# Kernel tuning notes

Hardware: AMD Instinct MI355X
Metric: run time of the kernel (lower is better)

The kernel has to match this reference:

```python
import jax, jax.numpy as jnp
import numpy as np

# Per-species MLP dims from CoefficientLayer._create_model (H, C, N, O), aev_dim=384
DIMS = {"h": [384, 160, 128, 96, 1], "c": [384, 144, 112, 96, 1], "n": [384, 128, 112, 96, 1], "o": [384, 128, 112, 96, 1]}


def setup_inputs() -> dict:
    key = jax.random.key(0)
    B, A, D = 256, 256, 384
    ks = jax.random.split(key, 64)
    inp = {}
    inp["species"] = jax.random.randint(ks[0], (B, A), 0, 4)  # species index 0..3
    inp["aev"] = jax.random.normal(ks[1], (B, A, D), dtype=jnp.float32)
    inp["b0"] = jnp.array([0.1, 0.2, 0.3, 0.4], dtype=jnp.float32)  # shifter intercepts
    inp["b1"] = jnp.array([1.0, 1.1, 0.9, 1.2], dtype=jnp.float32)  # shifter slopes
    ki = 2
    for name, dims in DIMS.items():
        for l in range(4):
            fi, fo = dims[l], dims[l + 1]
            inp[f"{name}w{l}"] = jax.random.normal(ks[ki], (fi, fo), dtype=jnp.float32) / np.float32(np.sqrt(fi))
            ki += 1
            inp[f"{name}b{l}"] = jnp.zeros((fo,), dtype=jnp.float32)
    return inp


def _mlp(x, ws, bs):
    # Linear -> CELU(0.1) x3 -> Linear(->1), squeeze last dim
    for i in range(3):
        x = jax.nn.celu(x @ ws[i] + bs[i], alpha=0.1)
    return (x @ ws[3] + bs[3])[..., 0]


def reference(species, aev, b0, b1,
              hw0, hb0, hw1, hb1, hw2, hb2, hw3, hb3,
              cw0, cb0, cw1, cb1, cw2, cb2, cw3, cb3,
              nw0, nb0, nw1, nb1, nw2, nb2, nw3, nb3,
              ow0, ob0, ow1, ob1, ow2, ob2, ow3, ob3):
    nets = [
        ([hw0, hw1, hw2, hw3], [hb0, hb1, hb2, hb3]),
        ([cw0, cw1, cw2, cw3], [cb0, cb1, cb2, cb3]),
        ([nw0, nw1, nw2, nw3], [nb0, nb1, nb2, nb3]),
        ([ow0, ow1, ow2, ow3], [ob0, ob1, ob2, ob3]),
    ]
    # ANIModel hard routing: each atom's coefficient comes from its species' network;
    # atoms with species == -1 (padding) stay 0.
    coef = jnp.zeros(species.shape, dtype=aev.dtype)
    for i, (ws, bs) in enumerate(nets):  # fixed small loop over 4 species
        coef = jnp.where(species == i, _mlp(aev, ws, bs), coef)
    # Shifter: result[mask_i] = b0[i] + b1[i] * coef[mask_i]; padding stays 0
    idx = jnp.clip(species, 0)
    return jnp.where(species >= 0, b0[idx] + b1[idx] * coef, jnp.zeros((), dtype=aev.dtype))
```

## Files before the change

kernel.cpp:

```cpp
#include <hip/hip_runtime.h>

typedef _Float16 f16;
typedef _Float16 f16x4 __attribute__((ext_vector_type(4)));
typedef _Float16 f16x8 __attribute__((ext_vector_type(8)));
typedef float f32x4 __attribute__((ext_vector_type(4)));
typedef unsigned short u16;
typedef unsigned int u32;

#define NATOMS 65536
#define CAP 17920

#define WS_LISTS_OFF 256
#define WS_W_OFF 524544
#define WS_W_ELEMS 350208
#define WS_NEEDED (WS_W_OFF + WS_W_ELEMS * 2)

#define BLKF 64

#define ROWB 1536
#define ROWH 768
#define TILEH 12288

struct ConvJob { const float* src; int K, N, KS, NT, CK, off; };

struct PrepParams {
  const int* species;
  int* counts;
  u16* lists;
  f16* wbase;
  ConvJob jobs[16];
};

struct GemmParams {
  const float* aev;
  const float* b0;
  const float* b1;
  const float* bias[4][4];
  const float* w3src[4];
  const f16* w[4][4];
  const int* counts;
  const u16* lists;
  float* out;
  int Nreal0[4];
  int Nreal1[4];
};

template <int N> struct AF { f16x8 v[N]; };

__global__ __launch_bounds__(256) void prep_kernel(PrepParams p) {
  int tid = threadIdx.x;
  if (blockIdx.x < 256) {
    __shared__ int wcnt[4][4];
    __shared__ int wbase[4][4];
    int i = blockIdx.x * 256 + tid;
    int s = p.species[i];
    int wave = tid >> 6, lane = tid & 63;
    unsigned long long m[4];
    #pragma unroll
    for (int t = 0; t < 4; t++) {
      m[t] = __ballot(s == t);
      if (lane == 0) wcnt[wave][t] = __popcll(m[t]);
    }
    __syncthreads();
    if (tid < 4) {
      int t = tid;
      int c0 = wcnt[0][t], c1 = wcnt[1][t], c2 = wcnt[2][t], c3 = wcnt[3][t];
      int base = atomicAdd(&p.counts[t], c0 + c1 + c2 + c3);
      wbase[0][t] = base;
      wbase[1][t] = base + c0;
      wbase[2][t] = base + c0 + c1;
      wbase[3][t] = base + c0 + c1 + c2;
    }
    __syncthreads();
    int rnk = __popcll(m[s] & ((1ull << lane) - 1ull));
    p.lists[s * NATOMS + wbase[wave][s] + rnk] = (u16)i;
  } else {
    int bx = blockIdx.x - 256;
    int job = bx / 30, bxin = bx - job * 30;
    ConvJob jb = p.jobs[job];
    int e = bxin * 256 + tid;
    int nslots = jb.KS * jb.NT * 64;
    if (e >= nslots) return;
    int frag = e >> 6, lane = e & 63;
    int c = frag / (jb.CK * jb.NT);
    int rem = frag - c * (jb.CK * jb.NT);
    int ckc = min(jb.CK, jb.KS - c * jb.CK);
    int nt = rem / ckc, ki = rem - nt * ckc;
    int ks = c * jb.CK + ki;
    int q = lane >> 4, nlo = lane & 15;
    int n = nt * 16 + nlo;
    int k0 = ks * 32 + q * 8;
    f16x8 v;
    #pragma unroll
    for (int j = 0; j < 8; j++) {
      int k = k0 + j;
      float x = (n < jb.N && k < jb.K) ? jb.src[k * jb.N + n] : 0.f;
      v[j] = (f16)x;
    }
    *(f16x8*)(p.wbase + jb.off + (size_t)e * 8) = v;
  }
}

__device__ __forceinline__ float celu01(float v) {
  return v > 0.f ? v : 0.1f * (__expf(v * 10.f) - 1.f);
}

__device__ __forceinline__ void stage_frag(const f16* g, f16* l, int lane) {
  __builtin_amdgcn_global_load_lds(
      (const __attribute__((address_space(1))) u32*)(g + lane * 8),
      (__attribute__((address_space(3))) u32*)l, 16, 0, 0);
}

template <int NT0, int KS1>
__device__ void fused_body(const GemmParams& p, int s, int bl, char* smem) {
  constexpr int LDSA_OFF = 4 * TILEH;
  constexpr int TSTRIDE = 16 * 168;
  constexpr int W1_OFF = LDSA_OFF + 8 * TSTRIDE * 2;
  constexpr int W2_OFF = W1_OFF + 40 * 512 * 2;
  constexpr int ATOMS_OFF = W2_OFF + 24 * 512 * 2;
  constexpr int NF1 = KS1 * 8;

  int tid = threadIdx.x, w = tid >> 6, lane = tid & 63;
  int q = lane >> 4, nlo = lane & 15;
  int cnt = min(p.counts[s], CAP);
  int ntiles = (cnt + 15) >> 4;
  int tpb = (ntiles + BLKF - 1) / BLKF;
  int t0 = bl * tpb;
  int nt_blk = min(ntiles - t0, tpb);
  if (nt_blk <= 0) return;

  f16* ldsA = (f16*)(smem + LDSA_OFF);
  f16* W1 = (f16*)(smem + W1_OFF);
  f16* W2 = (f16*)(smem + W2_OFF);
  u16* atoms_l = (u16*)(smem + ATOMS_OFF);

  const f16* g1 = p.w[s][1];
  const f16* g2 = p.w[s][2];
  for (int f = w; f < NF1 + 24; f += 10) {
    if (f < NF1) stage_frag(g1 + (size_t)f * 512, W1 + f * 512, lane);
    else stage_frag(g2 + (size_t)(f - NF1) * 512, W2 + (f - NF1) * 512, lane);
  }

  f16x8 wf[12];
  float bvv[4];
  if (w < NT0) {
    const f16* wg = p.w[s][0];
    #pragma unroll
    for (int ks = 0; ks < 12; ks++)
      wf[ks] = *(const f16x8*)(wg + (size_t)(ks * NT0 + w) * 512 + lane * 8);
    #pragma unroll
    for (int r = 0; r < 4; r++) {
      int n = w * 16 + q * 4 + r;
      bvv[r] = (n < p.Nreal0[s]) ? p.bias[s][0][n] : 0.f;
    }
  }

  int Nr1 = p.Nreal1[s];
  const float* bias1 = p.bias[s][1];
  const float* bias2 = p.bias[s][2];
  const float* w3 = p.w3src[s];
  float bv1[8], b2v[6], w3v[6];
  #pragma unroll
  for (int nt = 0; nt < 8; nt++) {
    int n = nt * 16 + nlo;
    bv1[nt] = (n < Nr1) ? bias1[n] : 0.f;
  }
  #pragma unroll
  for (int nt = 0; nt < 6; nt++) {
    int n = nt * 16 + nlo;
    b2v[nt] = bias2[n];
    w3v[nt] = w3[n];
  }
  float b3 = p.bias[s][3][0];
  float b0v = p.b0[s], b1v = p.b1[s];

  const u16* list = p.lists + s * NATOMS;
  for (int idx = tid; idx < nt_blk * 16; idx += 640)
    atoms_l[idx] = list[min(t0 * 16 + idx, cnt - 1)];
  __syncthreads();

  bool stager = (w < 8);
  int frow[3], fintra[3];
  #pragma unroll
  for (int j = 0; j < 3; j++) {
    int o32 = (w + 8 * j) * 1024 + lane * 16;
    frow[j] = o32 / ROWB;
    fintra[j] = o32 - frow[j] * ROWB;
  }

  f32x4 ldA[3], ldB[3];
  auto issueA = [&](int i) {
    #pragma unroll
    for (int j = 0; j < 3; j++) {
      int atom = atoms_l[i * 16 + frow[j]];
      ldA[j] = *(const f32x4*)((const char*)p.aev + (size_t)atom * ROWB + fintra[j]);
    }
  };
  auto issueB = [&](int i) {
    #pragma unroll
    for (int j = 0; j < 3; j++) {
      int atom = atoms_l[i * 16 + frow[j]];
      ldB[j] = *(const f32x4*)((const char*)p.aev + (size_t)atom * ROWB + fintra[j]);
    }
  };
  auto writeA = [&](int i) {
    char* buf = smem + (i & 3) * TILEH;
    #pragma unroll
    for (int j = 0; j < 3; j++) {
      int o16 = (w + 8 * j) * 512 + lane * 8;
      int addr = o16 ^ ((frow[j] & 7) << 4);
      f16x4 h = {(f16)ldA[j][0], (f16)ldA[j][1], (f16)ldA[j][2], (f16)ldA[j][3]};
      *(f16x4*)(buf + addr) = h;
    }
  };
  auto writeB = [&](int i) {
    char* buf = smem + (i & 3) * TILEH;
    #pragma unroll
    for (int j = 0; j < 3; j++) {
      int o16 = (w + 8 * j) * 512 + lane * 8;
      int addr = o16 ^ ((frow[j] & 7) << 4);
      f16x4 h = {(f16)ldB[j][0], (f16)ldB[j][1], (f16)ldB[j][2], (f16)ldB[j][3]};
      *(f16x4*)(buf + addr) = h;
    }
  };
  auto computeT = [&](int i, int lo) {
    const char* buf = smem + (i & 3) * TILEH;
    int swz = (nlo & 7) << 4;
    int base = nlo * ROWH + q * 16;
    f32x4 acc = {0.f, 0.f, 0.f, 0.f};
    #pragma unroll
    for (int ks = 0; ks < 12; ks++) {
      f16x8 a = *(const f16x8*)(buf + ((base + ks * 64) ^ swz));
      acc = __builtin_amdgcn_mfma_f32_16x16x32_f16(wf[ks], a, acc, 0, 0, 0);
    }
    f16* A = ldsA + (i - lo) * TSTRIDE;
    f16x4 o;
    #pragma unroll
    for (int r = 0; r < 4; r++) o[r] = (f16)celu01(acc[r] + bvv[r]);
    *(f16x4*)(A + nlo * 168 + w * 16 + q * 4) = o;
  };

  for (int lo = 0; lo < nt_blk; lo += 8) {
    int hi = min(nt_blk, lo + 8);

    if (stager) {
      issueA(lo);
      if (lo + 1 < hi) issueB(lo + 1);
      writeA(lo);
      if (lo + 1 < hi) writeB(lo + 1);
      if (lo + 2 < hi) issueA(lo + 2);
      if (lo + 3 < hi) issueB(lo + 3);
    }
    asm volatile("s_waitcnt lgkmcnt(0)" ::: "memory");
    __builtin_amdgcn_s_barrier();

    for (int i = lo; i < hi; i += 2) {
      if (stager) {
        if (i + 2 < hi) writeA(i + 2);
        if (i + 3 < hi) writeB(i + 3);
        if (i + 4 < hi) issueA(i + 4);
        if (i + 5 < hi) issueB(i + 5);
      }
      if (w < NT0) {
        computeT(i, lo);
        if (i + 1 < hi) computeT(i + 1, lo);
      }
      asm volatile("s_waitcnt lgkmcnt(0)" ::: "memory");
      __builtin_amdgcn_s_barrier();
    }

    if (w < 8 && lo + w < hi) {
      int i = lo + w;
      f16* A = ldsA + w * TSTRIDE;
      AF<KS1> a1;
      #pragma unroll
      for (int ks = 0; ks < KS1; ks++)
        a1.v[ks] = *(const f16x8*)(A + nlo * 168 + ks * 32 + q * 8);
      f32x4 acc1[8];
      #pragma unroll
      for (int nt = 0; nt < 8; nt++) acc1[nt] = f32x4{0.f, 0.f, 0.f, 0.f};
      #pragma unroll
      for (int ks = 0; ks < KS1; ks++) {
        #pragma unroll
        for (int nt = 0; nt < 8; nt++) {
          f16x8 b = *(const f16x8*)(W1 + (ks * 8 + nt) * 512 + lane * 8);
          acc1[nt] = __builtin_amdgcn_mfma_f32_16x16x32_f16(a1.v[ks], b, acc1[nt], 0, 0, 0);
        }
      }
      #pragma unroll
      for (int nt = 0; nt < 8; nt++) {
        #pragma unroll
        for (int r = 0; r < 4; r++)
          A[(q * 4 + r) * 168 + nt * 16 + nlo] = (f16)celu01(acc1[nt][r] + bv1[nt]);
      }
      AF<4> a2;
      #pragma unroll
      for (int ks = 0; ks < 4; ks++)
        a2.v[ks] = *(const f16x8*)(A + nlo * 168 + ks * 32 + q * 8);
      f32x4 acc2[6];
      #pragma unroll
      for (int nt = 0; nt < 6; nt++) acc2[nt] = f32x4{0.f, 0.f, 0.f, 0.f};
      #pragma unroll
      for (int ks = 0; ks < 4; ks++) {
        #pragma unroll
        for (int nt = 0; nt < 6; nt++) {
          f16x8 b = *(const f16x8*)(W2 + (ks * 6 + nt) * 512 + lane * 8);
          acc2[nt] = __builtin_amdgcn_mfma_f32_16x16x32_f16(a2.v[ks], b, acc2[nt], 0, 0, 0);
        }
      }
      float pr[4] = {0.f, 0.f, 0.f, 0.f};
      #pragma unroll
      for (int nt = 0; nt < 6; nt++) {
        #pragma unroll
        for (int r = 0; r < 4; r++) {
          float v = celu01(acc2[nt][r] + b2v[nt]);
          pr[r] += v * w3v[nt];
        }
      }
      #pragma unroll
      for (int m = 1; m < 16; m <<= 1) {
        #pragma unroll
        for (int r = 0; r < 4; r++) pr[r] += __shfl_xor(pr[r], m);
      }
      if (nlo == 0) {
        #pragma unroll
        for (int r = 0; r < 4; r++) {
          int row = (t0 + i) * 16 + q * 4 + r;
          if (row < cnt)
            p.out[atoms_l[i * 16 + q * 4 + r]] = b0v + b1v * (pr[r] + b3);
        }
      }
    }
    asm volatile("s_waitcnt lgkmcnt(0)" ::: "memory");
    __builtin_amdgcn_s_barrier();
  }
}

__global__ __launch_bounds__(640, 2) void fused_kernel(GemmParams p) {
  __shared__ __align__(16) char smem[158208];
  int s = blockIdx.x & 3, bl = blockIdx.x >> 2;
  switch (s) {
    case 0: fused_body<10, 5>(p, 0, bl, smem); break;
    case 1: fused_body<10, 5>(p, 1, bl, smem); break;
    case 2: fused_body<8, 4>(p, 2, bl, smem); break;
    default: fused_body<8, 4>(p, 3, bl, smem); break;
  }
}


extern "C" void kernel_launch(void* const* d_in, const int* in_sizes, int n_in,
                              void* d_out, int out_size, void* d_ws, size_t ws_size,
                              hipStream_t stream) {
  if (ws_size < WS_NEEDED) return;

  const int* species = (const int*)d_in[0];
  const float* aev = (const float*)d_in[1];
  const float* b0 = (const float*)d_in[2];
  const float* b1 = (const float*)d_in[3];

  static const int F1[4]  = {160, 144, 128, 128};
  static const int F1p[4] = {160, 160, 128, 128};
  static const int F2[4]  = {128, 112, 112, 112};

  char* wsb = (char*)d_ws;
  int* counts = (int*)wsb;
  u16* lists = (u16*)(wsb + WS_LISTS_OFF);
  f16* wbase = (f16*)(wsb + WS_W_OFF);

  PrepParams pp;
  pp.species = species; pp.counts = counts; pp.lists = lists; pp.wbase = wbase;

  GemmParams mp;
  mp.aev = aev; mp.b0 = b0; mp.b1 = b1;
  mp.counts = counts; mp.lists = lists; mp.out = (float*)d_out;

  int off = 0, ji = 0;
  for (int s = 0; s < 4; s++) {
    int K[4]  = {384, F1[s], F2[s], 96};
    int N[4]  = {F1[s], F2[s], 96, 1};
    int KS[4] = {12, F1p[s] / 32, 4, 3};
    int NT[4] = {F1p[s] / 16, 8, 6, 1};
    int CK[4] = {1, 1, 1, 3};
    for (int l = 0; l < 4; l++) {
      const float* w = (const float*)d_in[4 + s * 8 + l * 2];
      const float* b = (const float*)d_in[4 + s * 8 + l * 2 + 1];
      pp.jobs[ji].src = w;
      pp.jobs[ji].K = K[l];
      pp.jobs[ji].N = N[l];
      pp.jobs[ji].KS = KS[l];
      pp.jobs[ji].NT = NT[l];
      pp.jobs[ji].CK = CK[l];
      pp.jobs[ji].off = off;
      mp.w[s][l] = wbase + off;
      mp.bias[s][l] = b;
      off += KS[l] * NT[l] * 512;
      ji++;
    }
    mp.w3src[s] = (const float*)d_in[4 + s * 8 + 6];
    mp.Nreal0[s] = F1[s];
    mp.Nreal1[s] = F2[s];
  }

  hipMemsetAsync(d_ws, 0, 64, stream);
  prep_kernel<<<dim3(256 + 480), 256, 0, stream>>>(pp);
  fused_kernel<<<dim3(4 * BLKF), 640, 0, stream>>>(mp);
}
```

Measured before the change: 259.0 us.

## Switch aev staging to double-buffered LDS with three-deep register prefetch

```diff
diff --git a/kernel.cpp b/kernel.cpp
--- a/kernel.cpp
+++ b/kernel.cpp
@@ -113,7 +113,7 @@
 
 template <int NT0, int KS1>
 __device__ void fused_body(const GemmParams& p, int s, int bl, char* smem) {
-  constexpr int LDSA_OFF = 4 * TILEH;
+  constexpr int LDSA_OFF = 2 * TILEH;
   constexpr int TSTRIDE = 16 * 168;
   constexpr int W1_OFF = LDSA_OFF + 8 * TSTRIDE * 2;
   constexpr int W2_OFF = W1_OFF + 40 * 512 * 2;
@@ -188,7 +188,7 @@
     fintra[j] = o32 - frow[j] * ROWB;
   }
 
-  f32x4 ldA[3], ldB[3];
+  f32x4 ldA[3], ldB[3], ldC[3];
   auto issueA = [&](int i) {
     #pragma unroll
     for (int j = 0; j < 3; j++) {
@@ -203,8 +203,15 @@
       ldB[j] = *(const f32x4*)((const char*)p.aev + (size_t)atom * ROWB + fintra[j]);
     }
   };
+  auto issueC = [&](int i) {
+    #pragma unroll
+    for (int j = 0; j < 3; j++) {
+      int atom = atoms_l[i * 16 + frow[j]];
+      ldC[j] = *(const f32x4*)((const char*)p.aev + (size_t)atom * ROWB + fintra[j]);
+    }
+  };
   auto writeA = [&](int i) {
-    char* buf = smem + (i & 3) * TILEH;
+    char* buf = smem + (i & 1) * TILEH;
     #pragma unroll
     for (int j = 0; j < 3; j++) {
       int o16 = (w + 8 * j) * 512 + lane * 8;
@@ -214,7 +221,7 @@
     }
   };
   auto writeB = [&](int i) {
-    char* buf = smem + (i & 3) * TILEH;
+    char* buf = smem + (i & 1) * TILEH;
     #pragma unroll
     for (int j = 0; j < 3; j++) {
       int o16 = (w + 8 * j) * 512 + lane * 8;
@@ -223,8 +230,18 @@
       *(f16x4*)(buf + addr) = h;
     }
   };
+  auto writeC = [&](int i) {
+    char* buf = smem + (i & 1) * TILEH;
+    #pragma unroll
+    for (int j = 0; j < 3; j++) {
+      int o16 = (w + 8 * j) * 512 + lane * 8;
+      int addr = o16 ^ ((frow[j] & 7) << 4);
+      f16x4 h = {(f16)ldC[j][0], (f16)ldC[j][1], (f16)ldC[j][2], (f16)ldC[j][3]};
+      *(f16x4*)(buf + addr) = h;
+    }
+  };
   auto computeT = [&](int i, int lo) {
-    const char* buf = smem + (i & 3) * TILEH;
+    const char* buf = smem + (i & 1) * TILEH;
     int swz = (nlo & 7) << 4;
     int base = nlo * ROWH + q * 16;
     f32x4 acc = {0.f, 0.f, 0.f, 0.f};
@@ -242,32 +259,36 @@
 
   for (int lo = 0; lo < nt_blk; lo += 8) {
     int hi = min(nt_blk, lo + 8);
+    int n = hi - lo;
 
     if (stager) {
       issueA(lo);
-      if (lo + 1 < hi) issueB(lo + 1);
+      if (n > 1) issueB(lo + 1);
+      if (n > 2) issueC(lo + 2);
       writeA(lo);
-      if (lo + 1 < hi) writeB(lo + 1);
-      if (lo + 2 < hi) issueA(lo + 2);
-      if (lo + 3 < hi) issueB(lo + 3);
     }
     asm volatile("s_waitcnt lgkmcnt(0)" ::: "memory");
     __builtin_amdgcn_s_barrier();
 
-    for (int i = lo; i < hi; i += 2) {
-      if (stager) {
-        if (i + 2 < hi) writeA(i + 2);
-        if (i + 3 < hi) writeB(i + 3);
-        if (i + 4 < hi) issueA(i + 4);
-        if (i + 5 < hi) issueB(i + 5);
-      }
-      if (w < NT0) {
-        computeT(i, lo);
-        if (i + 1 < hi) computeT(i + 1, lo);
-      }
-      asm volatile("s_waitcnt lgkmcnt(0)" ::: "memory");
-      __builtin_amdgcn_s_barrier();
-    }
+    #define BODY(ii, WSET, ISET)                                    \
+    if (ii < n) {                                                   \
+      if (stager) {                                                 \
+        if (ii + 3 < n) ISET(lo + ii + 3);                          \
+        if (ii + 1 < n) WSET(lo + ii + 1);                          \
+      }                                                             \
+      if (w < NT0) computeT(lo + ii, lo);                           \
+      asm volatile("s_waitcnt lgkmcnt(0)" ::: "memory");            \
+      __builtin_amdgcn_s_barrier();                                 \
+    }
+    BODY(0, writeB, issueA)
+    BODY(1, writeC, issueB)
+    BODY(2, writeA, issueC)
+    BODY(3, writeB, issueA)
+    BODY(4, writeC, issueB)
+    BODY(5, writeA, issueC)
+    BODY(6, writeB, issueA)
+    BODY(7, writeC, issueB)
+    #undef BODY
 
     if (w < 8 && lo + w < hi) {
       int i = lo + w;
@@ -337,7 +358,7 @@
 }
 
 __global__ __launch_bounds__(640, 2) void fused_kernel(GemmParams p) {
-  __shared__ __align__(16) char smem[158208];
+  __shared__ __align__(16) char smem[133760];
   int s = blockIdx.x & 3, bl = blockIdx.x >> 2;
   switch (s) {
     case 0: fused_body<10, 5>(p, 0, bl, smem); break;
```

Result: slower. 264.6 us (+2.2%).
